# Performance work log

Hardware: AMD Instinct MI355X
Metric: run time of the kernel (lower is better)

Reference implementation:

```python
import jax, jax.numpy as jnp
import numpy as np

WINDOW = 8
HEADS = 16
HIDDEN = 256
EMBED = HIDDEN * WINDOW          # 2048
HEAD_DIM = EMBED // HEADS        # 128
BATCH = 8
SEQ = 4096                       # multiple of WINDOW
GROUP = SEQ // WINDOW            # 512


def _indices():
    # index_one[i*g + j] = j*w + i  (residue-class grouping permutation)
    i = np.arange(WINDOW)
    j = np.arange(GROUP)
    index_one = (j[None, :] * WINDOW + i[:, None]).reshape(-1)
    # index_two[i*w + k] = k*g + i  (inverse-style interleave permutation)
    index_two = (np.arange(WINDOW)[None, :] * GROUP + np.arange(GROUP)[:, None]).reshape(-1)
    return jnp.asarray(index_one), jnp.asarray(index_two)


def _attention(M, Wq, Wk, Wv, fc_w, fc_b):
    # M: [N, g, E] with E = heads*head_dim
    N, L, E = M.shape
    x = M.reshape(N, L, HEADS, HEAD_DIM)
    q = jnp.einsum('nlhd,ed->nlhe', x, Wq)
    k = jnp.einsum('nlhd,ed->nlhe', x, Wk)
    v = jnp.einsum('nlhd,ed->nlhe', x, Wv)
    energy = jnp.einsum('nqhd,nkhd->nhqk', q, k)
    attn = jax.nn.softmax(energy / jnp.sqrt(jnp.float32(EMBED)), axis=-1)
    out = jnp.einsum('nhqk,nkhd->nqhd', attn, v).reshape(N, L, E)
    return out @ fc_w.T + fc_b


def setup_inputs() -> dict:
    key = jax.random.key(0)
    ks = jax.random.split(key, 6)
    s = 0.02
    return {
        'M': jax.random.normal(ks[0], (BATCH, SEQ, HIDDEN), jnp.float32),
        'Wq': jax.random.normal(ks[1], (HEAD_DIM, HEAD_DIM), jnp.float32) * s,
        'Wk': jax.random.normal(ks[2], (HEAD_DIM, HEAD_DIM), jnp.float32) * s,
        'Wv': jax.random.normal(ks[3], (HEAD_DIM, HEAD_DIM), jnp.float32) * s,
        'fc_w': jax.random.normal(ks[4], (EMBED, EMBED), jnp.float32) * s,
        'fc_b': jax.random.normal(ks[5], (EMBED,), jnp.float32) * s,
        'device': 0,
    }


def reference(M, Wq, Wk, Wv, fc_w, fc_b, device):
    del device  # unused, mirrors torch signature
    index_one, index_two = _indices()
    N, S, H = M.shape
    w, g = WINDOW, GROUP
    for b in range(w):
        idx = (index_one - b) % S
        M = M[:, idx]                                             # gather permute
        # segmentation step 1: [N, w*g, H] -> [N, g, w*H]
        M = M.reshape(N, w, g, H).transpose(0, 2, 1, 3).reshape(N, g, w * H)
        M = _attention(M, Wq, Wk, Wv, fc_w, fc_b)
        # segmentation step 2: [N, g, w*H] -> [N, w*g, H]
        M = M.reshape(N, g, w, H).transpose(0, 2, 1, 3).reshape(N, w * g, H)
        # index_two rotated once per iteration after the first -> roll by -b
        M = M[:, jnp.roll(index_two, -b)]
    return M[:, :S]
```

## Files before the change

kernel.cpp:

```cpp
#include <hip/hip_runtime.h>
#include <stdint.h>

typedef unsigned short u16;
typedef unsigned int u32;
typedef __bf16 bf16x8 __attribute__((ext_vector_type(8)));
typedef float f32x4 __attribute__((ext_vector_type(4)));
typedef float f32x16 __attribute__((ext_vector_type(16)));
typedef u16 u16x4 __attribute__((ext_vector_type(4)));
typedef u16 u16x8 __attribute__((ext_vector_type(8)));

#define MFMA16(a, b, c) __builtin_amdgcn_mfma_f32_16x16x32_bf16(a, b, c, 0, 0, 0)
#define MFMA32(a, b, c) __builtin_amdgcn_mfma_f32_32x32x16_bf16(a, b, c, 0, 0, 0)

__device__ __forceinline__ u16 f2bf(float f) {
  u32 u = __builtin_bit_cast(u32, f);
  u += 0x7FFFu + ((u >> 16) & 1u);
  return (u16)(u >> 16);
}

__device__ __forceinline__ bf16x8 ld16(const u16* p) {
  return __builtin_bit_cast(bf16x8, *(const uint4*)p);
}

__device__ __forceinline__ void gl_lds(const u16* src, u16* lds) {
  __builtin_amdgcn_global_load_lds(
      (const __attribute__((address_space(1))) u32*)src,
      (__attribute__((address_space(3))) u32*)lds, 16, 0, 0);
}

__global__ __launch_bounds__(256) void convert_weights(
    const float* __restrict__ Wq, const float* __restrict__ Wk,
    const float* __restrict__ Wv, const float* __restrict__ fcw,
    const float* __restrict__ M, u16* __restrict__ wq_b,
    u16* __restrict__ wk_b, u16* __restrict__ wv_b, u16* __restrict__ fcw_b,
    u16* __restrict__ Sb) {
  int bx = blockIdx.x, tid = threadIdx.x;
  if (bx < 4096) {
    int i = (bx * 256 + tid) * 4;
    float4 f = *(const float4*)&fcw[i];
    u16x4 o = {f2bf(f.x), f2bf(f.y), f2bf(f.z), f2bf(f.w)};
    *(u16x4*)&fcw_b[i] = o;
  } else if (bx < 4112) {
    int i = ((bx - 4096) * 256 + tid) * 4;
    const float sc = 0.022097086912079612f;
    float4 q = *(const float4*)&Wq[i];
    u16x4 oq = {f2bf(q.x * sc), f2bf(q.y * sc), f2bf(q.z * sc), f2bf(q.w * sc)};
    *(u16x4*)&wq_b[i] = oq;
    float4 k = *(const float4*)&Wk[i];
    u16x4 ok = {f2bf(k.x), f2bf(k.y), f2bf(k.z), f2bf(k.w)};
    *(u16x4*)&wk_b[i] = ok;
    float4 v = *(const float4*)&Wv[i];
    u16x4 ov = {f2bf(v.x), f2bf(v.y), f2bf(v.z), f2bf(v.w)};
    *(u16x4*)&wv_b[i] = ov;
  } else {
    size_t i = ((size_t)(bx - 4112) * 256 + tid) * 8;
    float4 f0 = *(const float4*)&M[i];
    float4 f1 = *(const float4*)&M[i + 4];
    u16x8 v = {f2bf(f0.x), f2bf(f0.y), f2bf(f0.z), f2bf(f0.w),
               f2bf(f1.x), f2bf(f1.y), f2bf(f1.z), f2bf(f1.w)};
    *(u16x8*)&Sb[i] = v;
  }
}

__global__ __launch_bounds__(512) void kv_kernel(
    const u16* __restrict__ srcB, const u16* __restrict__ wk,
    const u16* __restrict__ wvw, u16* __restrict__ K, u16* __restrict__ Vt,
    int bsh) {
  __shared__ u16 X[64 * 264];
  int jt = blockIdx.x, i0 = blockIdx.y, n = blockIdx.z;
  int tid = threadIdx.x;
#pragma unroll
  for (int it = 0; it < 4; ++it) {
    int c = tid + it * 512;
    int row = c >> 5, seg = c & 31;
    int pos = (8 * (jt * 64 + row) + i0 - bsh) & 4095;
    size_t base = ((size_t)n * 4096 + pos) * 256 + seg * 8;
    *(u16x8*)&X[row * 264 + seg * 8] = *(const u16x8*)&srcB[base];
  }
  __syncthreads();
  int wvid = tid >> 6, ln = tid & 63;
  int mat = wvid >> 2, hc = wvid & 3;
  int hh = hc >> 1, cb = (hc & 1) * 64;
  int h = i0 * 2 + hh, xc = hh * 128;
  const u16* W = (mat == 0) ? wk : wvw;
  int lr = ln & 15, lg = ln >> 4;
  f32x4 acc[4][4] = {};
#pragma unroll
  for (int kt = 0; kt < 4; ++kt) {
    bf16x8 a[4], b[4];
#pragma unroll
    for (int mt = 0; mt < 4; ++mt)
      a[mt] = ld16(&X[(mt * 16 + lr) * 264 + xc + kt * 32 + lg * 8]);
#pragma unroll
    for (int nc = 0; nc < 4; ++nc)
      b[nc] = ld16(&W[(cb + nc * 16 + lr) * 128 + kt * 32 + lg * 8]);
#pragma unroll
    for (int mt = 0; mt < 4; ++mt)
#pragma unroll
      for (int nc = 0; nc < 4; ++nc)
        acc[mt][nc] = MFMA16(a[mt], b[nc], acc[mt][nc]);
  }
  size_t nh = (size_t)(n * 16 + h);
  if (mat == 0) {
    u16* dst = K + nh * 512 * 128;
#pragma unroll
    for (int mt = 0; mt < 4; ++mt)
#pragma unroll
      for (int nc = 0; nc < 4; ++nc) {
        int col = cb + nc * 16 + lr;
        int jb = jt * 64 + mt * 16 + lg * 4;
#pragma unroll
        for (int r = 0; r < 4; ++r)
          dst[(size_t)(jb + r) * 128 + col] = f2bf(acc[mt][nc][r]);
      }
  } else {
    u16* dst = Vt + nh * 128 * 512;
#pragma unroll
    for (int mt = 0; mt < 4; ++mt)
#pragma unroll
      for (int nc = 0; nc < 4; ++nc) {
        int col = cb + nc * 16 + lr;
        int jb = jt * 64 + mt * 16 + lg * 4;
        u16x4 pk = {f2bf(acc[mt][nc][0]), f2bf(acc[mt][nc][1]),
                    f2bf(acc[mt][nc][2]), f2bf(acc[mt][nc][3])};
        *(u16x4*)&dst[(size_t)col * 512 + jb] = pk;
      }
  }
}

__global__ __launch_bounds__(256, 2) void attn_kernel(
    const u16* __restrict__ Sb, const u16* __restrict__ wq,
    const u16* __restrict__ K, const u16* __restrict__ Vt,
    u16* __restrict__ O, int bsh) {
  __shared__ u16 SMEM[40960];
#define KLp(b) (&SMEM[(b) * 8192])
#define VLp(b) (&SMEM[24576 + (b) * 8192])
  int flat = blockIdx.x;
  int xcd = flat & 7, idx = flat >> 3;
  int gl = idx & 15, qt = idx >> 4;
  int g = xcd | (gl << 3);
  int h = g & 15, n = g >> 4;
  int tid = threadIdx.x, wv = tid >> 6, ln = tid & 63;
  int l31 = ln & 31, hh = ln >> 5;
  size_t nh = (size_t)(n * 16 + h);
  int q0 = qt * 128 + wv * 32;
  const u16* Kb = K + (size_t)nh * 512 * 128;
  const u16* Vb = Vt + (size_t)nh * 128 * 512;
  int i0h = h >> 1, c0 = (h & 1) * 128;

  int l16 = ln & 15, l8 = ln & 7;
  int rK[4], cK[4], rV[4], cV[4];
#pragma unroll
  for (int i = 0; i < 4; ++i) {
    int s = wv * 4 + i;
    rK[i] = 4 * s + (ln >> 4);
    cK[i] = (l16 ^ (rK[i] & 15)) * 8;
    rV[i] = 8 * s + (ln >> 3);
    cV[i] = (l8 ^ (rV[i] & 7)) * 8;
  }

#define STAGE_K(buf, kv)                                                     \
  {                                                                          \
    const u16* kp_ = Kb + (size_t)(kv) * 64 * 128;                           \
    _Pragma("unroll") for (int i_ = 0; i_ < 4; ++i_) {                       \
      int s_ = wv * 4 + i_;                                                  \
      gl_lds(&kp_[(size_t)rK[i_] * 128 + cK[i_]], &KLp(buf)[s_ * 512]);      \
    }                                                                        \
  }
#define STAGE_V(buf, kv)                                                     \
  {                                                                          \
    _Pragma("unroll") for (int i_ = 0; i_ < 4; ++i_) {                       \
      int s_ = wv * 4 + i_;                                                  \
      gl_lds(&Vb[(size_t)rV[i_] * 512 + (kv)*64 + cV[i_]], &VLp(buf)[s_ * 512]); \
    }                                                                        \
  }

#pragma unroll
  for (int i = 0; i < 8; ++i) {
    int s = wv * 8 + i;
    int r = 4 * s + (ln >> 4);
    int slot = (ln & 15) ^ (r & 15);
    int pos = (8 * (qt * 128 + r) + i0h - bsh) & 4095;
    gl_lds(&Sb[((size_t)n * 4096 + pos) * 256 + c0 + slot * 8], &SMEM[s * 512]);
    gl_lds(&wq[r * 128 + slot * 8], &SMEM[16384 + s * 512]);
  }
  STAGE_V(1, 0);
  __syncthreads();
  f32x16 qd[4] = {};
  int jr = wv * 32 + l31;
#pragma unroll
  for (int cs = 0; cs < 8; ++cs) {
    bf16x8 xf = ld16(&SMEM[jr * 128 + ((2 * cs + hh) ^ (jr & 15)) * 8]);
#pragma unroll
    for (int eb = 0; eb < 4; ++eb) {
      int er = eb * 32 + l31;
      bf16x8 wf = ld16(&SMEM[16384 + er * 128 + ((2 * cs + hh) ^ (er & 15)) * 8]);
      qd[eb] = MFMA32(wf, xf, qd[eb]);
    }
  }
  bf16x8 qf[8];
#pragma unroll
  for (int kt = 0; kt < 8; ++kt) {
    const int eb = kt >> 1, r0 = 8 * (kt & 1);
    u32 wA, wB, wC, wD;
    asm("v_cvt_pk_bf16_f32 %0, %1, %2" : "=v"(wA) : "v"(qd[eb][r0 + 0]), "v"(qd[eb][r0 + 1]));
    asm("v_cvt_pk_bf16_f32 %0, %1, %2" : "=v"(wB) : "v"(qd[eb][r0 + 2]), "v"(qd[eb][r0 + 3]));
    asm("v_cvt_pk_bf16_f32 %0, %1, %2" : "=v"(wC) : "v"(qd[eb][r0 + 4]), "v"(qd[eb][r0 + 5]));
    asm("v_cvt_pk_bf16_f32 %0, %1, %2" : "=v"(wD) : "v"(qd[eb][r0 + 6]), "v"(qd[eb][r0 + 7]));
    asm("v_permlane32_swap_b32 %0, %1" : "+v"(wA), "+v"(wC));
    asm("v_permlane32_swap_b32 %0, %1" : "+v"(wB), "+v"(wD));
    uint4 ww = {wA, wB, wC, wD};
    qf[kt] = __builtin_bit_cast(bf16x8, ww);
  }
  __syncthreads();

  STAGE_K(0, 0);
  STAGE_K(1, 1);
  __syncthreads();

  f32x16 o[4] = {};
  float m = -1e30f, l = 0.f;

#pragma unroll
  for (int t = 0; t < 8; ++t) {
    if (t < 7) STAGE_V(t & 1, t + 1);
    if (t < 6) STAGE_K((t + 2) % 3, t + 2);
    f32x16 s[2] = {};
#pragma unroll
    for (int kt = 0; kt < 8; ++kt) {
      int slot0 = (2 * kt + hh) ^ (l31 & 15);
      bf16x8 a0 = ld16(&KLp(t % 3)[l31 * 128 + slot0 * 8]);
      s[0] = MFMA32(a0, qf[kt], s[0]);
      int row1 = 32 + l31;
      int slot1 = (2 * kt + hh) ^ (row1 & 15);
      bf16x8 a1 = ld16(&KLp(t % 3)[row1 * 128 + slot1 * 8]);
      s[1] = MFMA32(a1, qf[kt], s[1]);
    }
    float mx[8];
#pragma unroll
    for (int i = 0; i < 8; ++i)
      mx[i] = fmaxf(fmaxf(s[0][2 * i], s[0][2 * i + 1]),
                    fmaxf(s[1][2 * i], s[1][2 * i + 1]));
    float pm = fmaxf(fmaxf(fmaxf(mx[0], mx[1]), fmaxf(mx[2], mx[3])),
                     fmaxf(fmaxf(mx[4], mx[5]), fmaxf(mx[6], mx[7])));
    pm = fmaxf(pm, __shfl_xor(pm, 32));
    if (!__all(pm <= m + 8.f)) {
      float nm = fmaxf(m, pm);
      float al = __expf(m - nm);
      l *= al;
      m = nm;
#pragma unroll
      for (int r = 0; r < 16; ++r) {
        int qr = (r & 3) + 8 * (r >> 2) + 4 * hh;
        float av = __shfl(al, (ln & 32) | qr, 64);
        o[0][r] *= av; o[1][r] *= av; o[2][r] *= av; o[3][r] *= av;
      }
    }
#pragma unroll
    for (int kb2 = 0; kb2 < 2; ++kb2)
#pragma unroll
      for (int r = 0; r < 16; ++r) s[kb2][r] = __expf(s[kb2][r] - m);
    float sm[8];
#pragma unroll
    for (int i = 0; i < 8; ++i)
      sm[i] = (s[0][2 * i] + s[0][2 * i + 1]) + (s[1][2 * i] + s[1][2 * i + 1]);
    float rs = ((sm[0] + sm[1]) + (sm[2] + sm[3])) +
               ((sm[4] + sm[5]) + (sm[6] + sm[7]));
    rs += __shfl_xor(rs, 32);
    l += rs;
    bf16x8 pa[4];
#pragma unroll
    for (int ks = 0; ks < 4; ++ks) {
      const int kb2 = ks >> 1, r0 = 8 * (ks & 1);
      u32 wA, wB, wC, wD;
      asm("v_cvt_pk_bf16_f32 %0, %1, %2" : "=v"(wA) : "v"(s[kb2][r0 + 0]), "v"(s[kb2][r0 + 1]));
      asm("v_cvt_pk_bf16_f32 %0, %1, %2" : "=v"(wB) : "v"(s[kb2][r0 + 2]), "v"(s[kb2][r0 + 3]));
      asm("v_cvt_pk_bf16_f32 %0, %1, %2" : "=v"(wC) : "v"(s[kb2][r0 + 4]), "v"(s[kb2][r0 + 5]));
      asm("v_cvt_pk_bf16_f32 %0, %1, %2" : "=v"(wD) : "v"(s[kb2][r0 + 6]), "v"(s[kb2][r0 + 7]));
      asm("v_permlane32_swap_b32 %0, %1" : "+v"(wA), "+v"(wC));
      asm("v_permlane32_swap_b32 %0, %1" : "+v"(wB), "+v"(wD));
      uint4 ww = {wA, wB, wC, wD};
      pa[ks] = __builtin_bit_cast(bf16x8, ww);
    }
    __builtin_amdgcn_s_setprio(1);
#pragma unroll
    for (int ks = 0; ks < 4; ++ks)
#pragma unroll
      for (int nb = 0; nb < 4; ++nb) {
        int row = nb * 32 + l31;
        int slot = (2 * ks + hh) ^ (row & 7);
        bf16x8 bv = ld16(&VLp((t + 1) & 1)[row * 64 + slot * 8]);
        o[nb] = MFMA32(pa[ks], bv, o[nb]);
      }
    __builtin_amdgcn_s_setprio(0);
    if (t < 6) {
      asm volatile("s_waitcnt vmcnt(4)" ::: "memory");
      __builtin_amdgcn_s_barrier();
    } else if (t == 6) {
      asm volatile("s_waitcnt vmcnt(0)" ::: "memory");
      __builtin_amdgcn_s_barrier();
    }
  }
#undef STAGE_K
#undef STAGE_V
#undef KLp
#undef VLp

  float inv = 1.f / l;
#pragma unroll
  for (int r = 0; r < 16; ++r) {
    int qr = (r & 3) + 8 * (r >> 2) + 4 * hh;
    float iv = __shfl(inv, (ln & 32) | qr, 64);
    int row = q0 + qr;
    u16* dst = O + ((size_t)n * 512 + row) * 2048 + h * 128;
    dst[0 * 32 + l31] = f2bf(o[0][r] * iv);
    dst[1 * 32 + l31] = f2bf(o[1][r] * iv);
    dst[2 * 32 + l31] = f2bf(o[2][r] * iv);
    dst[3 * 32 + l31] = f2bf(o[3][r] * iv);
  }
}

__global__ __launch_bounds__(512, 1) void fc_kernel(
    const u16* __restrict__ A, const u16* __restrict__ Bw,
    const float* __restrict__ bias, float* __restrict__ doutF,
    u16* __restrict__ doutB, int last, int bsh) {
  __shared__ u16 AL[3][256 * 64];
  __shared__ u16 BL[3][128 * 64];
  int blk = blockIdx.x;
  int xcd = blk & 7, j = blk >> 3;
  int bn = xcd * 2 + (j & 1), bm = j >> 1;
  int tid = threadIdx.x, wv = tid >> 6, ln = tid & 63;
  int lr = ln & 15, lg = ln >> 4;
  int R0 = bm * 256, C0 = bn * 128;
  int wr = (wv >> 1) * 64, wc = (wv & 1) * 64;
  const u16* gA[4];
  int sA[4];
  const u16* gB[2];
  int sB[2];
#pragma unroll
  for (int i = 0; i < 4; ++i) {
    int r = wv * 32 + i * 8 + (ln >> 3);
    int cs = ((ln & 7) ^ (r & 7)) * 8;
    gA[i] = A + (size_t)(R0 + r) * 2048 + cs;
    sA[i] = (wv * 32 + i * 8) * 64;
  }
#pragma unroll
  for (int i = 0; i < 2; ++i) {
    int r = wv * 16 + i * 8 + (ln >> 3);
    int cs = ((ln & 7) ^ (r & 7)) * 8;
    gB[i] = Bw + (size_t)(C0 + r) * 2048 + cs;
    sB[i] = (wv * 16 + i * 8) * 64;
  }
  int aoff[4][2], boff[4][2];
#pragma unroll
  for (int i = 0; i < 4; ++i) {
    int ra = wr + i * 16 + lr, rb = wc + i * 16 + lr;
#pragma unroll
    for (int kk = 0; kk < 2; ++kk) {
      aoff[i][kk] = ra * 64 + (((kk * 4 + lg) ^ (ra & 7)) * 8);
      boff[i][kk] = rb * 64 + (((kk * 4 + lg) ^ (rb & 7)) * 8);
    }
  }
  f32x4 acc[4][4] = {};

#define STAGE6(buf, k0)                          \
  {                                              \
    gl_lds(gA[0] + (k0), &AL[buf][sA[0]]);       \
    gl_lds(gA[1] + (k0), &AL[buf][sA[1]]);       \
    gl_lds(gA[2] + (k0), &AL[buf][sA[2]]);       \
    gl_lds(gA[3] + (k0), &AL[buf][sA[3]]);       \
    gl_lds(gB[0] + (k0), &BL[buf][sB[0]]);       \
    gl_lds(gB[1] + (k0), &BL[buf][sB[1]]);       \
  }

  STAGE6(0, 0);
  STAGE6(1, 64);
  asm volatile("s_waitcnt vmcnt(6)" ::: "memory");
  __builtin_amdgcn_s_barrier();

  for (int t = 0; t < 32; ++t) {
    int cur = t % 3, nx2 = (t + 2) % 3;
    int k2 = (t + 2) * 64;
    bf16x8 a0 = ld16(&AL[cur][aoff[0][0]]), a1 = ld16(&AL[cur][aoff[1][0]]);
    bf16x8 a2 = ld16(&AL[cur][aoff[2][0]]), a3 = ld16(&AL[cur][aoff[3][0]]);
    bf16x8 b0 = ld16(&BL[cur][boff[0][0]]), b1 = ld16(&BL[cur][boff[1][0]]);
    bf16x8 b2 = ld16(&BL[cur][boff[2][0]]), b3 = ld16(&BL[cur][boff[3][0]]);
    if (t < 30) {
      gl_lds(gA[0] + k2, &AL[nx2][sA[0]]);
      gl_lds(gA[1] + k2, &AL[nx2][sA[1]]);
      gl_lds(gB[0] + k2, &BL[nx2][sB[0]]);
    }
    __builtin_amdgcn_s_barrier();
    asm volatile("s_waitcnt lgkmcnt(0)" ::: "memory");
    __builtin_amdgcn_sched_barrier(0);
    __builtin_amdgcn_s_setprio(1);
    acc[0][0] = MFMA16(a0, b0, acc[0][0]);
    acc[0][1] = MFMA16(a0, b1, acc[0][1]);
    acc[0][2] = MFMA16(a0, b2, acc[0][2]);
    acc[0][3] = MFMA16(a0, b3, acc[0][3]);
    acc[1][0] = MFMA16(a1, b0, acc[1][0]);
    acc[1][1] = MFMA16(a1, b1, acc[1][1]);
    acc[1][2] = MFMA16(a1, b2, acc[1][2]);
    acc[1][3] = MFMA16(a1, b3, acc[1][3]);
    acc[2][0] = MFMA16(a2, b0, acc[2][0]);
    acc[2][1] = MFMA16(a2, b1, acc[2][1]);
    acc[2][2] = MFMA16(a2, b2, acc[2][2]);
    acc[2][3] = MFMA16(a2, b3, acc[2][3]);
    acc[3][0] = MFMA16(a3, b0, acc[3][0]);
    acc[3][1] = MFMA16(a3, b1, acc[3][1]);
    acc[3][2] = MFMA16(a3, b2, acc[3][2]);
    acc[3][3] = MFMA16(a3, b3, acc[3][3]);
    __builtin_amdgcn_s_setprio(0);
    __builtin_amdgcn_s_barrier();
    a0 = ld16(&AL[cur][aoff[0][1]]); a1 = ld16(&AL[cur][aoff[1][1]]);
    a2 = ld16(&AL[cur][aoff[2][1]]); a3 = ld16(&AL[cur][aoff[3][1]]);
    b0 = ld16(&BL[cur][boff[0][1]]); b1 = ld16(&BL[cur][boff[1][1]]);
    b2 = ld16(&BL[cur][boff[2][1]]); b3 = ld16(&BL[cur][boff[3][1]]);
    if (t < 30) {
      gl_lds(gA[2] + k2, &AL[nx2][sA[2]]);
      gl_lds(gA[3] + k2, &AL[nx2][sA[3]]);
      gl_lds(gB[1] + k2, &BL[nx2][sB[1]]);
      asm volatile("s_waitcnt vmcnt(6)" ::: "memory");
    } else if (t == 30) {
      asm volatile("s_waitcnt vmcnt(0)" ::: "memory");
    }
    __builtin_amdgcn_s_barrier();
    asm volatile("s_waitcnt lgkmcnt(0)" ::: "memory");
    __builtin_amdgcn_sched_barrier(0);
    __builtin_amdgcn_s_setprio(1);
    acc[0][0] = MFMA16(a0, b0, acc[0][0]);
    acc[0][1] = MFMA16(a0, b1, acc[0][1]);
    acc[0][2] = MFMA16(a0, b2, acc[0][2]);
    acc[0][3] = MFMA16(a0, b3, acc[0][3]);
    acc[1][0] = MFMA16(a1, b0, acc[1][0]);
    acc[1][1] = MFMA16(a1, b1, acc[1][1]);
    acc[1][2] = MFMA16(a1, b2, acc[1][2]);
    acc[1][3] = MFMA16(a1, b3, acc[1][3]);
    acc[2][0] = MFMA16(a2, b0, acc[2][0]);
    acc[2][1] = MFMA16(a2, b1, acc[2][1]);
    acc[2][2] = MFMA16(a2, b2, acc[2][2]);
    acc[2][3] = MFMA16(a2, b3, acc[2][3]);
    acc[3][0] = MFMA16(a3, b0, acc[3][0]);
    acc[3][1] = MFMA16(a3, b1, acc[3][1]);
    acc[3][2] = MFMA16(a3, b2, acc[3][2]);
    acc[3][3] = MFMA16(a3, b3, acc[3][3]);
    __builtin_amdgcn_s_setprio(0);
    __builtin_amdgcn_s_barrier();
  }
#undef STAGE6
#pragma unroll
  for (int nc = 0; nc < 4; ++nc) {
    int e = C0 + wc + nc * 16 + lr;
    float bv = bias[e];
    int i = e >> 8, cc = e & 255;
#pragma unroll
    for (int mt = 0; mt < 4; ++mt)
#pragma unroll
      for (int r = 0; r < 4; ++r) {
        int row = R0 + wr + mt * 16 + lg * 4 + r;
        int nn = row >> 9, jj = row & 511;
        int pos = (8 * jj + i - bsh) & 4095;
        size_t di = ((size_t)nn * 4096 + pos) * 256 + cc;
        float v = acc[mt][nc][r] + bv;
        if (last) doutF[di] = v;
        else doutB[di] = f2bf(v);
      }
  }
}

extern "C" void kernel_launch(void* const* d_in, const int* in_sizes, int n_in,
                              void* d_out, int out_size, void* d_ws, size_t ws_size,
                              hipStream_t stream) {
  const float* M = (const float*)d_in[0];
  const float* Wq = (const float*)d_in[1];
  const float* Wk = (const float*)d_in[2];
  const float* Wv = (const float*)d_in[3];
  const float* fcw = (const float*)d_in[4];
  const float* fcb = (const float*)d_in[5];
  float* out = (float*)d_out;
  char* ws = (char*)d_ws;
  u16* wq_b = (u16*)(ws + (0 << 10));
  u16* wk_b = (u16*)(ws + (32 << 10));
  u16* wv_b = (u16*)(ws + (64 << 10));
  u16* fcw_b = (u16*)(ws + (128 << 10));
  u16* Kb = (u16*)(ws + ((size_t)32 << 20));
  u16* Vtb = (u16*)(ws + ((size_t)48 << 20));
  u16* Ab = (u16*)(ws + ((size_t)64 << 20));
  u16* Sb = (u16*)(ws + ((size_t)96 << 20));

  convert_weights<<<8208, 256, 0, stream>>>(Wq, Wk, Wv, fcw, M, wq_b, wk_b,
                                            wv_b, fcw_b, Sb);
  for (int b = 0; b < 8; ++b) {
    kv_kernel<<<dim3(8, 8, 8), 512, 0, stream>>>(Sb, wk_b, wv_b, Kb, Vtb, b);
    attn_kernel<<<512, 256, 0, stream>>>(Sb, wq_b, Kb, Vtb, Ab, b);
    fc_kernel<<<256, 512, 0, stream>>>(Ab, fcw_b, fcb, out, Sb,
                                       (b == 7) ? 1 : 0, b);
  }
}
```

Baseline: 706.8 us.

## Widen attention blocks to 256 queries with 8 waves sharing K/V tiles

The attention kernel now runs 512 threads per block covering 256 query rows instead of 128, so each staged K/V tile in LDS serves twice as many waves. The grid halves to 256 blocks. Each wave stages half as many K/V chunks, and Wq is loaded in two halves so the larger Q-input tile still fits in shared memory. This trades extra barriers during Q projection and fewer blocks, possibly under-filling the CUs, for less redundant K/V global traffic.

```diff
diff --git a/kernel.cpp b/kernel.cpp
--- a/kernel.cpp
+++ b/kernel.cpp
@@ -128,7 +128,7 @@
   }
 }
 
-__global__ __launch_bounds__(256, 2) void attn_kernel(
+__global__ __launch_bounds__(512, 1) void attn_kernel(
     const u16* __restrict__ Sb, const u16* __restrict__ wq,
     const u16* __restrict__ K, const u16* __restrict__ Vt,
     u16* __restrict__ O, int bsh) {
@@ -137,54 +137,32 @@
 #define VLp(b) (&SMEM[24576 + (b) * 8192])
   int flat = blockIdx.x;
   int xcd = flat & 7, idx = flat >> 3;
-  int gl = idx & 15, qt = idx >> 4;
+  int gl = idx & 15, qtb = idx >> 4;
   int g = xcd | (gl << 3);
   int h = g & 15, n = g >> 4;
   int tid = threadIdx.x, wv = tid >> 6, ln = tid & 63;
   int l31 = ln & 31, hh = ln >> 5;
   size_t nh = (size_t)(n * 16 + h);
-  int q0 = qt * 128 + wv * 32;
+  int q0 = qtb * 256 + wv * 32;
   const u16* Kb = K + (size_t)nh * 512 * 128;
   const u16* Vb = Vt + (size_t)nh * 128 * 512;
   int i0h = h >> 1, c0 = (h & 1) * 128;
-
-  int l16 = ln & 15, l8 = ln & 7;
-  int rK[4], cK[4], rV[4], cV[4];
-#pragma unroll
-  for (int i = 0; i < 4; ++i) {
-    int s = wv * 4 + i;
-    rK[i] = 4 * s + (ln >> 4);
-    cK[i] = (l16 ^ (rK[i] & 15)) * 8;
-    rV[i] = 8 * s + (ln >> 3);
-    cV[i] = (l8 ^ (rV[i] & 7)) * 8;
-  }
-
-#define STAGE_K(buf, kv)                                                     \
-  {                                                                          \
-    const u16* kp_ = Kb + (size_t)(kv) * 64 * 128;                           \
-    _Pragma("unroll") for (int i_ = 0; i_ < 4; ++i_) {                       \
-      int s_ = wv * 4 + i_;                                                  \
-      gl_lds(&kp_[(size_t)rK[i_] * 128 + cK[i_]], &KLp(buf)[s_ * 512]);      \
-    }                                                                        \
-  }
-#define STAGE_V(buf, kv)                                                     \
-  {                                                                          \
-    _Pragma("unroll") for (int i_ = 0; i_ < 4; ++i_) {                       \
-      int s_ = wv * 4 + i_;                                                  \
-      gl_lds(&Vb[(size_t)rV[i_] * 512 + (kv)*64 + cV[i_]], &VLp(buf)[s_ * 512]); \
-    }                                                                        \
-  }
 
 #pragma unroll
   for (int i = 0; i < 8; ++i) {
     int s = wv * 8 + i;
     int r = 4 * s + (ln >> 4);
     int slot = (ln & 15) ^ (r & 15);
-    int pos = (8 * (qt * 128 + r) + i0h - bsh) & 4095;
+    int pos = (8 * (qtb * 256 + r) + i0h - bsh) & 4095;
     gl_lds(&Sb[((size_t)n * 4096 + pos) * 256 + c0 + slot * 8], &SMEM[s * 512]);
-    gl_lds(&wq[r * 128 + slot * 8], &SMEM[16384 + s * 512]);
-  }
-  STAGE_V(1, 0);
+  }
+#pragma unroll
+  for (int i = 0; i < 2; ++i) {
+    int s = wv * 2 + i;
+    int r = 4 * s + (ln >> 4);
+    int slot = (ln & 15) ^ (r & 15);
+    gl_lds(&wq[r * 128 + slot * 8], &SMEM[32768 + s * 512]);
+  }
   __syncthreads();
   f32x16 qd[4] = {};
   int jr = wv * 32 + l31;
@@ -192,9 +170,29 @@
   for (int cs = 0; cs < 8; ++cs) {
     bf16x8 xf = ld16(&SMEM[jr * 128 + ((2 * cs + hh) ^ (jr & 15)) * 8]);
 #pragma unroll
-    for (int eb = 0; eb < 4; ++eb) {
+    for (int eb = 0; eb < 2; ++eb) {
       int er = eb * 32 + l31;
-      bf16x8 wf = ld16(&SMEM[16384 + er * 128 + ((2 * cs + hh) ^ (er & 15)) * 8]);
+      bf16x8 wf = ld16(&SMEM[32768 + er * 128 + ((2 * cs + hh) ^ (er & 15)) * 8]);
+      qd[eb] = MFMA32(wf, xf, qd[eb]);
+    }
+  }
+  __syncthreads();
+#pragma unroll
+  for (int i = 0; i < 2; ++i) {
+    int s = wv * 2 + i;
+    int rg = 64 + 4 * s + (ln >> 4);
+    int slot = (ln & 15) ^ (rg & 15);
+    gl_lds(&wq[rg * 128 + slot * 8], &SMEM[32768 + s * 512]);
+  }
+  __syncthreads();
+#pragma unroll
+  for (int cs = 0; cs < 8; ++cs) {
+    bf16x8 xf = ld16(&SMEM[jr * 128 + ((2 * cs + hh) ^ (jr & 15)) * 8]);
+#pragma unroll
+    for (int eb = 2; eb < 4; ++eb) {
+      int erg = eb * 32 + l31;
+      int loc = erg - 64;
+      bf16x8 wf = ld16(&SMEM[32768 + loc * 128 + ((2 * cs + hh) ^ (erg & 15)) * 8]);
       qd[eb] = MFMA32(wf, xf, qd[eb]);
     }
   }
@@ -214,8 +212,35 @@
   }
   __syncthreads();
 
+  int rK[2], cK[2], rV[2], cV[2];
+#pragma unroll
+  for (int i = 0; i < 2; ++i) {
+    int s = wv * 2 + i;
+    rK[i] = 4 * s + (ln >> 4);
+    cK[i] = ((ln & 15) ^ (rK[i] & 15)) * 8;
+    rV[i] = 8 * s + (ln >> 3);
+    cV[i] = ((ln & 7) ^ (rV[i] & 7)) * 8;
+  }
+
+#define STAGE_K(buf, kv)                                                     \
+  {                                                                          \
+    const u16* kp_ = Kb + (size_t)(kv) * 64 * 128;                           \
+    _Pragma("unroll") for (int i_ = 0; i_ < 2; ++i_) {                       \
+      int s_ = wv * 2 + i_;                                                  \
+      gl_lds(&kp_[(size_t)rK[i_] * 128 + cK[i_]], &KLp(buf)[s_ * 512]);      \
+    }                                                                        \
+  }
+#define STAGE_V(buf, kv)                                                     \
+  {                                                                          \
+    _Pragma("unroll") for (int i_ = 0; i_ < 2; ++i_) {                       \
+      int s_ = wv * 2 + i_;                                                  \
+      gl_lds(&Vb[(size_t)rV[i_] * 512 + (kv)*64 + cV[i_]], &VLp(buf)[s_ * 512]); \
+    }                                                                        \
+  }
+
   STAGE_K(0, 0);
   STAGE_K(1, 1);
+  STAGE_V(1, 0);
   __syncthreads();
 
   f32x16 o[4] = {};
@@ -294,7 +319,7 @@
       }
     __builtin_amdgcn_s_setprio(0);
     if (t < 6) {
-      asm volatile("s_waitcnt vmcnt(4)" ::: "memory");
+      asm volatile("s_waitcnt vmcnt(2)" ::: "memory");
       __builtin_amdgcn_s_barrier();
     } else if (t == 6) {
       asm volatile("s_waitcnt vmcnt(0)" ::: "memory");
@@ -492,7 +517,7 @@
                                             wv_b, fcw_b, Sb);
   for (int b = 0; b < 8; ++b) {
     kv_kernel<<<dim3(8, 8, 8), 512, 0, stream>>>(Sb, wk_b, wv_b, Kb, Vtb, b);
-    attn_kernel<<<512, 256, 0, stream>>>(Sb, wq_b, Kb, Vtb, Ab, b);
+    attn_kernel<<<256, 512, 0, stream>>>(Sb, wq_b, Kb, Vtb, Ab, b);
     fc_kernel<<<256, 512, 0, stream>>>(Ab, fcw_b, fcb, out, Sb,
                                        (b == 7) ? 1 : 0, b);
   }
```

After: 670.8 us. -5.1%, faster.

## Double attention query tile per block and load X rows directly into registers

Applied to the files above, without the earlier changes.

The attention kernel now runs 512 threads covering 256 query rows per block, so each staged K/V tile serves twice as many queries and the grid is halved. Each wave loads its X rows for the Q projection straight from global memory into registers instead of staging them through LDS. K tile 0 is issued together with Wq and V before the first barrier, removing one synchronization. Per-thread staging loads drop from four to two, and the vmcnt waits are adjusted to match. The costs are fewer blocks in flight and reliance on one block per CU for latency hiding.

```diff
diff --git a/kernel.cpp b/kernel.cpp
--- a/kernel.cpp
+++ b/kernel.cpp
@@ -128,74 +128,78 @@
   }
 }
 
-__global__ __launch_bounds__(256, 2) void attn_kernel(
+__global__ __launch_bounds__(512, 1) void attn_kernel(
     const u16* __restrict__ Sb, const u16* __restrict__ wq,
     const u16* __restrict__ K, const u16* __restrict__ Vt,
     u16* __restrict__ O, int bsh) {
   __shared__ u16 SMEM[40960];
 #define KLp(b) (&SMEM[(b) * 8192])
 #define VLp(b) (&SMEM[24576 + (b) * 8192])
+#define WQB 8192
   int flat = blockIdx.x;
   int xcd = flat & 7, idx = flat >> 3;
-  int gl = idx & 15, qt = idx >> 4;
+  int gl = idx & 15, qtb = idx >> 4;
   int g = xcd | (gl << 3);
   int h = g & 15, n = g >> 4;
   int tid = threadIdx.x, wv = tid >> 6, ln = tid & 63;
   int l31 = ln & 31, hh = ln >> 5;
   size_t nh = (size_t)(n * 16 + h);
-  int q0 = qt * 128 + wv * 32;
+  int q0 = qtb * 256 + wv * 32;
   const u16* Kb = K + (size_t)nh * 512 * 128;
   const u16* Vb = Vt + (size_t)nh * 128 * 512;
   int i0h = h >> 1, c0 = (h & 1) * 128;
 
-  int l16 = ln & 15, l8 = ln & 7;
-  int rK[4], cK[4], rV[4], cV[4];
-#pragma unroll
-  for (int i = 0; i < 4; ++i) {
-    int s = wv * 4 + i;
+  int rK[2], cK[2], rV[2], cV[2];
+#pragma unroll
+  for (int i = 0; i < 2; ++i) {
+    int s = wv * 2 + i;
     rK[i] = 4 * s + (ln >> 4);
-    cK[i] = (l16 ^ (rK[i] & 15)) * 8;
+    cK[i] = ((ln & 15) ^ (rK[i] & 15)) * 8;
     rV[i] = 8 * s + (ln >> 3);
-    cV[i] = (l8 ^ (rV[i] & 7)) * 8;
+    cV[i] = ((ln & 7) ^ (rV[i] & 7)) * 8;
   }
 
 #define STAGE_K(buf, kv)                                                     \
   {                                                                          \
     const u16* kp_ = Kb + (size_t)(kv) * 64 * 128;                           \
-    _Pragma("unroll") for (int i_ = 0; i_ < 4; ++i_) {                       \
-      int s_ = wv * 4 + i_;                                                  \
+    _Pragma("unroll") for (int i_ = 0; i_ < 2; ++i_) {                       \
+      int s_ = wv * 2 + i_;                                                  \
       gl_lds(&kp_[(size_t)rK[i_] * 128 + cK[i_]], &KLp(buf)[s_ * 512]);      \
     }                                                                        \
   }
 #define STAGE_V(buf, kv)                                                     \
   {                                                                          \
-    _Pragma("unroll") for (int i_ = 0; i_ < 4; ++i_) {                       \
-      int s_ = wv * 4 + i_;                                                  \
+    _Pragma("unroll") for (int i_ = 0; i_ < 2; ++i_) {                       \
+      int s_ = wv * 2 + i_;                                                  \
       gl_lds(&Vb[(size_t)rV[i_] * 512 + (kv)*64 + cV[i_]], &VLp(buf)[s_ * 512]); \
     }                                                                        \
   }
 
 #pragma unroll
-  for (int i = 0; i < 8; ++i) {
-    int s = wv * 8 + i;
-    int r = 4 * s + (ln >> 4);
-    int slot = (ln & 15) ^ (r & 15);
-    int pos = (8 * (qt * 128 + r) + i0h - bsh) & 4095;
-    gl_lds(&Sb[((size_t)n * 4096 + pos) * 256 + c0 + slot * 8], &SMEM[s * 512]);
-    gl_lds(&wq[r * 128 + slot * 8], &SMEM[16384 + s * 512]);
-  }
+  for (int i = 0; i < 4; ++i) {
+    int s = wv * 4 + i;
+    int rw = 4 * s + (ln >> 4);
+    int slot = (ln & 15) ^ (rw & 15);
+    gl_lds(&wq[rw * 128 + slot * 8], &SMEM[WQB + s * 512]);
+  }
+  STAGE_K(0, 0);
   STAGE_V(1, 0);
   __syncthreads();
+
+  int jr = wv * 32 + l31;
+  int posx = (8 * (qtb * 256 + jr) + i0h - bsh) & 4095;
+  const u16* xrow = Sb + ((size_t)n * 4096 + posx) * 256 + c0 + hh * 8;
+  bf16x8 xf[8];
+#pragma unroll
+  for (int cs = 0; cs < 8; ++cs) xf[cs] = ld16(&xrow[cs * 16]);
   f32x16 qd[4] = {};
-  int jr = wv * 32 + l31;
 #pragma unroll
   for (int cs = 0; cs < 8; ++cs) {
-    bf16x8 xf = ld16(&SMEM[jr * 128 + ((2 * cs + hh) ^ (jr & 15)) * 8]);
 #pragma unroll
     for (int eb = 0; eb < 4; ++eb) {
       int er = eb * 32 + l31;
-      bf16x8 wf = ld16(&SMEM[16384 + er * 128 + ((2 * cs + hh) ^ (er & 15)) * 8]);
-      qd[eb] = MFMA32(wf, xf, qd[eb]);
+      bf16x8 wf = ld16(&SMEM[WQB + er * 128 + ((2 * cs + hh) ^ (er & 15)) * 8]);
+      qd[eb] = MFMA32(wf, xf[cs], qd[eb]);
     }
   }
   bf16x8 qf[8];
@@ -214,9 +218,7 @@
   }
   __syncthreads();
 
-  STAGE_K(0, 0);
   STAGE_K(1, 1);
-  __syncthreads();
 
   f32x16 o[4] = {};
   float m = -1e30f, l = 0.f;
@@ -294,7 +296,7 @@
       }
     __builtin_amdgcn_s_setprio(0);
     if (t < 6) {
-      asm volatile("s_waitcnt vmcnt(4)" ::: "memory");
+      asm volatile("s_waitcnt vmcnt(2)" ::: "memory");
       __builtin_amdgcn_s_barrier();
     } else if (t == 6) {
       asm volatile("s_waitcnt vmcnt(0)" ::: "memory");
@@ -305,6 +307,7 @@
 #undef STAGE_V
 #undef KLp
 #undef VLp
+#undef WQB
 
   float inv = 1.f / l;
 #pragma unroll
@@ -492,7 +495,7 @@
                                             wv_b, fcw_b, Sb);
   for (int b = 0; b < 8; ++b) {
     kv_kernel<<<dim3(8, 8, 8), 512, 0, stream>>>(Sb, wk_b, wv_b, Kb, Vtb, b);
-    attn_kernel<<<512, 256, 0, stream>>>(Sb, wq_b, Kb, Vtb, Ab, b);
+    attn_kernel<<<256, 512, 0, stream>>>(Sb, wq_b, Kb, Vtb, Ab, b);
     fc_kernel<<<256, 512, 0, stream>>>(Ab, fcw_b, fcb, out, Sb,
                                        (b == 7) ? 1 : 0, b);
   }
```

Result: faster. 665.0 us (median of 2 runs) (-5.9%).
